# Performance work log

Measured on AMD Instinct MI355X. Metric: run time of the kernel, lower is better.

Reference implementation:

```python
import jax, jax.numpy as jnp
import numpy as np

B, N, C, H, W = 32, 8, 256, 4, 4


def setup_inputs() -> dict:
    key = jax.random.key(0)
    k1, k2 = jax.random.split(key)
    pred = jax.random.normal(k1, (B, N, C, H, W), dtype=jnp.float32)
    gt = jax.random.normal(k2, (B, N, C, H, W), dtype=jnp.float32)
    return {"pred": pred, "gt": gt}


def reference(pred, gt):
    b, n, c, h, w = pred.shape
    M = b * n * h * w
    # (B,N,C,H,W) -> (B,N,H,W,C) -> (M, C)
    p = jnp.transpose(pred, (0, 1, 3, 4, 2)).reshape(M, c)
    # (B,N,C,H,W) -> (C,B,N,H,W) -> (C, M)
    g = jnp.transpose(gt, (2, 0, 1, 3, 4)).reshape(c, M)
    lossmat = p @ g  # (M, M) similarity matrix
    # CrossEntropy with target = arange(M): -mean(log_softmax diag)
    logp = jax.nn.log_softmax(lossmat, axis=1)
    loss = -jnp.mean(jnp.diagonal(logp))
    # accuracy (no grad in original)
    top1 = jnp.argmax(lossmat, axis=1)
    acc = jnp.mean((top1 == jnp.arange(M)).astype(jnp.float32)) * 100.0
    return (loss, acc)
```

## Files before the change

### kernel.cpp

```cpp
#include <hip/hip_runtime.h>
#include <cstdint>

typedef __bf16 bf16x8 __attribute__((ext_vector_type(8)));
typedef float floatx4 __attribute__((ext_vector_type(4)));


#define OFF_X     (0u)
#define OFF_Y     (2u*1024*1024)
#define OFF_PMAX  (4u*1024*1024)
#define OFF_PSUM  (5u*1024*1024)
#define OFF_DIAG  (6u*1024*1024)
#define OFF_LPART (OFF_DIAG + 16384u)
#define OFF_CPART (OFF_LPART + 256u)
#define OFF_CNT   (OFF_CPART + 256u)

#define AS1C(p) ((const __attribute__((address_space(1))) void*)(const void*)(p))
#define AS3(p)  ((__attribute__((address_space(3))) void*)(void*)(p))

__global__ __launch_bounds__(256) void transpose_stage(
    const float* __restrict__ pred, const float* __restrict__ gt,
    unsigned short* __restrict__ Xs, unsigned short* __restrict__ Ys,
    int* __restrict__ cnt) {
  int blk = blockIdx.x;
  const int t = threadIdx.x;
  if (blk == 0 && t < 33) cnt[t] = 0;
  const float* src;
  unsigned short* dst;
  int slab;
  if (blk < 256) { src = pred; dst = Xs; slab = blk; }
  else           { src = gt;   dst = Ys; slab = blk - 256; }
  const float* sb = src + slab * 4096;
  const int rb = slab >> 3, rowhi = slab & 7;
  #pragma unroll
  for (int half = 0; half < 2; ++half) {
    int c_ = half * 256 + t;
    int rowlo = c_ & 15;
    int quad  = (c_ >> 4) & 3;
    int kk    = (c_ >> 6) & 1;
    int s     = c_ >> 7;
    int k0 = s * 64 + kk * 32 + quad * 8;
    unsigned int packed[4];
    #pragma unroll
    for (int jj = 0; jj < 4; ++jj) {
      unsigned int lohi[2];
      #pragma unroll
      for (int e = 0; e < 2; ++e) {
        float f = sb[(k0 + jj * 2 + e) * 16 + rowlo];
        unsigned int u = __float_as_uint(f);
        lohi[e] = (u + 0x7FFFu + ((u >> 16) & 1u)) >> 16;
      }
      packed[jj] = lohi[0] | (lohi[1] << 16);
    }
    unsigned short* o = dst + rb * 32768 +
        (unsigned)(s * 1024 + kk * 512 + rowhi * 64 + quad * 16 + rowlo) * 8;
    uint4 v; v.x = packed[0]; v.y = packed[1]; v.z = packed[2]; v.w = packed[3];
    *reinterpret_cast<uint4*>(o) = v;
  }
}

__global__ __launch_bounds__(512) void gemm_softmax_partial(
    const unsigned short* __restrict__ Xs, const unsigned short* __restrict__ Ys,
    float* __restrict__ pmax, float* __restrict__ psum, float* __restrict__ diag) {
  __shared__ __align__(16) unsigned short As[2][16384];
  __shared__ __align__(16) unsigned short Bs[2][16384];
  const int t = threadIdx.x;
  const int wave = t >> 6, lane = t & 63;
  const int rg = wave >> 2, cg = wave & 3;
  const int h = blockIdx.x;
  const int xcd = h & 7, slot = h >> 3;
  const int bR = ((xcd >> 1) << 2) | (slot & 3);
  const int bC = ((xcd & 1) << 3) | (slot >> 2);
  const unsigned short* Ag = Xs + bR * 65536;
  const unsigned short* Bg = Ys + bC * 65536;

  floatx4 acc[8][4];
  const floatx4 zero = {0.f, 0.f, 0.f, 0.f};
  #pragma unroll
  for (int i = 0; i < 8; ++i)
    #pragma unroll
    for (int j = 0; j < 4; ++j) acc[i][j] = zero;

#define STAGE(BUF, S) do {                                                   \
    _Pragma("unroll") for (int it = 0; it < 4; ++it) {                       \
      int chunk = it * 512 + t;                                 \
      int half = chunk >> 10, w_ = chunk & 1023;                             \
      __builtin_amdgcn_global_load_lds(                                      \
          AS1C(Ag + half * 32768 + (S) * 8192 + w_ * 8),                     \
          AS3(&As[BUF][(unsigned)chunk * 8]), 16, 0, 0);                     \
      __builtin_amdgcn_global_load_lds(                                      \
          AS1C(Bg + half * 32768 + (S) * 8192 + w_ * 8),                     \
          AS3(&Bs[BUF][(unsigned)chunk * 8]), 16, 0, 0);                     \
    }                                                                        \
  } while (0)

#define COMPUTE(BUF) do {                                                    \
    _Pragma("unroll") for (int kk = 0; kk < 2; ++kk) {                       \
      bf16x8 b[4];                                                           \
      _Pragma("unroll") for (int fc = 0; fc < 4; ++fc) {                     \
        int gc = cg * 4 + fc;                                                \
        b[fc] = *reinterpret_cast<const bf16x8*>(                            \
            &Bs[BUF][(unsigned)((gc >> 3) * 8192 + kk * 4096 +               \
                                (gc & 7) * 512 + lane * 8)]);                \
      }                                                                      \
      _Pragma("unroll") for (int fr = 0; fr < 8; ++fr) {                     \
        bf16x8 a = *reinterpret_cast<const bf16x8*>(                         \
            &As[BUF][(unsigned)(rg * 8192 + kk * 4096 + fr * 512 +           \
                                lane * 8)]);                                 \
        _Pragma("unroll") for (int fc = 0; fc < 4; ++fc)                     \
          acc[fr][fc] = __builtin_amdgcn_mfma_f32_16x16x32_bf16(             \
              a, b[fc], acc[fr][fc], 0, 0, 0);                               \
      }                                                                      \
    }                                                                        \
  } while (0)

#define BAR_ACQ(N) do {                                                      \
    asm volatile("s_waitcnt vmcnt(" #N ")" ::: "memory");                    \
    __builtin_amdgcn_s_barrier();                                            \
    asm volatile("" ::: "memory");                                           \
  } while (0)
#define BAR_REL() do {                                                       \
    asm volatile("" ::: "memory");                                           \
    __builtin_amdgcn_s_barrier();                                            \
  } while (0)

  STAGE(0, 0);
  STAGE(1, 1);
  BAR_ACQ(8);
  COMPUTE(0);
  BAR_REL();
  STAGE(0, 2);
  BAR_ACQ(8);
  COMPUTE(1);
  BAR_REL();
  STAGE(1, 3);
  BAR_ACQ(8);
  COMPUTE(0);
  BAR_ACQ(0);
  COMPUTE(1);

#undef STAGE
#undef COMPUTE
#undef BAR_ACQ
#undef BAR_REL

  const int quad = lane >> 4, lc = lane & 15;

  if (bR == bC) {
    #pragma unroll
    for (int fr = 0; fr < 8; ++fr) {
      if (cg == 2 * rg + (fr >> 2)) {
        #pragma unroll
        for (int r = 0; r < 4; ++r)
          if (lc == quad * 4 + r)
            diag[bR * 256 + rg * 128 + fr * 16 + lc] = acc[fr][fr & 3][r];
      }
    }
  }

  #pragma unroll
  for (int fr = 0; fr < 8; ++fr) {
    #pragma unroll
    for (int r = 0; r < 4; ++r) {
      float v0 = acc[fr][0][r], v1 = acc[fr][1][r];
      float v2 = acc[fr][2][r], v3 = acc[fr][3][r];
      float m = fmaxf(fmaxf(v0, v1), fmaxf(v2, v3));
      #pragma unroll
      for (int sh = 1; sh < 16; sh <<= 1) m = fmaxf(m, __shfl_xor(m, sh, 64));
      float ss = __expf(v0 - m) + __expf(v1 - m) +
                 __expf(v2 - m) + __expf(v3 - m);
      #pragma unroll
      for (int sh = 1; sh < 16; sh <<= 1) ss += __shfl_xor(ss, sh, 64);
      if (lc == 0) {
        int grow = bR * 256 + rg * 128 + fr * 16 + quad * 4 + r;
        int p = grow * 64 + bC * 4 + cg;
        pmax[p] = m; psum[p] = ss;
      }
    }
  }
}

__global__ __launch_bounds__(256) void combine_rows(
    const float* __restrict__ pmax, const float* __restrict__ psum,
    const float* __restrict__ diag,
    float* __restrict__ lpart, float* __restrict__ cpart,
    int* __restrict__ cnt, float* __restrict__ out) {
  int row = blockIdx.x * 256 + threadIdx.x;
  const float* pm = pmax + row * 64;
  const float* ps = psum + row * 64;
  float M = -3.4e38f;
  #pragma unroll 8
  for (int b = 0; b < 64; ++b) M = fmaxf(M, pm[b]);
  float S = 0.f;
  #pragma unroll 8
  for (int b = 0; b < 64; ++b) S += ps[b] * __expf(pm[b] - M);
  float d = diag[row];
  float lossr = logf(S) + M - d;
  float corr = (d == M) ? 1.f : 0.f;
  #pragma unroll
  for (int sh = 1; sh < 64; sh <<= 1) {
    lossr += __shfl_xor(lossr, sh, 64);
    corr  += __shfl_xor(corr,  sh, 64);
  }
  __shared__ float ls[4], cs[4];
  int wave = threadIdx.x >> 6, lane = threadIdx.x & 63;
  if (lane == 0) { ls[wave] = lossr; cs[wave] = corr; }
  __syncthreads();
  if (threadIdx.x == 0) {
    lpart[blockIdx.x] = ls[0] + ls[1] + ls[2] + ls[3];
    cpart[blockIdx.x] = cs[0] + cs[1] + cs[2] + cs[3];
    __threadfence();
    if (atomicAdd(cnt, 1) == 15) {
      __threadfence();
      float L = 0.f, C = 0.f;
      for (int i = 0; i < 16; ++i) { L += lpart[i]; C += cpart[i]; }
      out[0] = L * (1.f / 4096.f);
      out[1] = C * (100.f / 4096.f);
    }
  }
}

extern "C" void kernel_launch(void* const* d_in, const int* in_sizes, int n_in,
                              void* d_out, int out_size, void* d_ws, size_t ws_size,
                              hipStream_t stream) {
  const float* pred = (const float*)d_in[0];
  const float* gt   = (const float*)d_in[1];
  char* w = (char*)d_ws;
  unsigned short* Xbf = (unsigned short*)(w + OFF_X);
  unsigned short* Ybf = (unsigned short*)(w + OFF_Y);
  float* pmax  = (float*)(w + OFF_PMAX);
  float* psum  = (float*)(w + OFF_PSUM);
  float* diag  = (float*)(w + OFF_DIAG);
  float* lpart = (float*)(w + OFF_LPART);
  float* cpart = (float*)(w + OFF_CPART);
  int*   cnt   = (int*)(w + OFF_CNT);
  float* out   = (float*)d_out;

  transpose_stage<<<512, 256, 0, stream>>>(pred, gt, Xbf, Ybf, cnt);
  gemm_softmax_partial<<<256, 512, 0, stream>>>(Xbf, Ybf, pmax, psum, diag);
  combine_rows<<<16, 256, 0, stream>>>(pmax, psum, diag, lpart, cpart, cnt, out);
}
```

Baseline: 94.20 us.

## Materialize full similarity matrix and compute softmax in separate combine kernel

The GEMM kernel no longer fuses the per-tile row max/sum-exp reduction. It writes the full 4096x4096 fp32 logits matrix to workspace. A new combine kernel streams each row to compute the max, log-sum-exp, diagonal and argmax match, and a tiny finalize kernel replaces the atomic-counter last-block reduction. This removes shuffle-heavy epilogue work from the GEMM but adds a 64 MB global write and read plus an extra launch.

```diff
diff --git a/kernel.cpp b/kernel.cpp
--- a/kernel.cpp
+++ b/kernel.cpp
@@ -7,23 +7,18 @@
 
 #define OFF_X     (0u)
 #define OFF_Y     (2u*1024*1024)
-#define OFF_PMAX  (4u*1024*1024)
-#define OFF_PSUM  (5u*1024*1024)
-#define OFF_DIAG  (6u*1024*1024)
-#define OFF_LPART (OFF_DIAG + 16384u)
-#define OFF_CPART (OFF_LPART + 256u)
-#define OFF_CNT   (OFF_CPART + 256u)
+#define OFF_LPART (4u*1024*1024)
+#define OFF_CPART (4u*1024*1024 + 4096u)
+#define OFF_LM    (16u*1024*1024)
 
 #define AS1C(p) ((const __attribute__((address_space(1))) void*)(const void*)(p))
 #define AS3(p)  ((__attribute__((address_space(3))) void*)(void*)(p))
 
 __global__ __launch_bounds__(256) void transpose_stage(
     const float* __restrict__ pred, const float* __restrict__ gt,
-    unsigned short* __restrict__ Xs, unsigned short* __restrict__ Ys,
-    int* __restrict__ cnt) {
+    unsigned short* __restrict__ Xs, unsigned short* __restrict__ Ys) {
   int blk = blockIdx.x;
   const int t = threadIdx.x;
-  if (blk == 0 && t < 33) cnt[t] = 0;
   const float* src;
   unsigned short* dst;
   int slab;
@@ -58,9 +53,9 @@
   }
 }
 
-__global__ __launch_bounds__(512) void gemm_softmax_partial(
+__global__ __launch_bounds__(512) void gemm_c(
     const unsigned short* __restrict__ Xs, const unsigned short* __restrict__ Ys,
-    float* __restrict__ pmax, float* __restrict__ psum, float* __restrict__ diag) {
+    float* __restrict__ LM) {
   __shared__ __align__(16) unsigned short As[2][16384];
   __shared__ __align__(16) unsigned short Bs[2][16384];
   const int t = threadIdx.x;
@@ -144,78 +139,71 @@
 #undef BAR_REL
 
   const int quad = lane >> 4, lc = lane & 15;
-
-  if (bR == bC) {
-    #pragma unroll
-    for (int fr = 0; fr < 8; ++fr) {
-      if (cg == 2 * rg + (fr >> 2)) {
-        #pragma unroll
-        for (int r = 0; r < 4; ++r)
-          if (lc == quad * 4 + r)
-            diag[bR * 256 + rg * 128 + fr * 16 + lc] = acc[fr][fr & 3][r];
-      }
-    }
-  }
-
-  #pragma unroll
-  for (int fr = 0; fr < 8; ++fr) {
-    #pragma unroll
-    for (int r = 0; r < 4; ++r) {
-      float v0 = acc[fr][0][r], v1 = acc[fr][1][r];
-      float v2 = acc[fr][2][r], v3 = acc[fr][3][r];
-      float m = fmaxf(fmaxf(v0, v1), fmaxf(v2, v3));
+  float* Cb = LM + (size_t)(bR * 256 + rg * 128 + quad * 4) * 4096 +
+              bC * 256 + cg * 64 + lc;
+  #pragma unroll
+  for (int fr = 0; fr < 8; ++fr)
+    #pragma unroll
+    for (int r = 0; r < 4; ++r)
       #pragma unroll
-      for (int sh = 1; sh < 16; sh <<= 1) m = fmaxf(m, __shfl_xor(m, sh, 64));
-      float ss = __expf(v0 - m) + __expf(v1 - m) +
-                 __expf(v2 - m) + __expf(v3 - m);
-      #pragma unroll
-      for (int sh = 1; sh < 16; sh <<= 1) ss += __shfl_xor(ss, sh, 64);
-      if (lc == 0) {
-        int grow = bR * 256 + rg * 128 + fr * 16 + quad * 4 + r;
-        int p = grow * 64 + bC * 4 + cg;
-        pmax[p] = m; psum[p] = ss;
-      }
-    }
-  }
-}
-
-__global__ __launch_bounds__(256) void combine_rows(
-    const float* __restrict__ pmax, const float* __restrict__ psum,
-    const float* __restrict__ diag,
-    float* __restrict__ lpart, float* __restrict__ cpart,
-    int* __restrict__ cnt, float* __restrict__ out) {
-  int row = blockIdx.x * 256 + threadIdx.x;
-  const float* pm = pmax + row * 64;
-  const float* ps = psum + row * 64;
-  float M = -3.4e38f;
-  #pragma unroll 8
-  for (int b = 0; b < 64; ++b) M = fmaxf(M, pm[b]);
-  float S = 0.f;
-  #pragma unroll 8
-  for (int b = 0; b < 64; ++b) S += ps[b] * __expf(pm[b] - M);
-  float d = diag[row];
-  float lossr = logf(S) + M - d;
-  float corr = (d == M) ? 1.f : 0.f;
-  #pragma unroll
-  for (int sh = 1; sh < 64; sh <<= 1) {
-    lossr += __shfl_xor(lossr, sh, 64);
-    corr  += __shfl_xor(corr,  sh, 64);
+      for (int fc = 0; fc < 4; ++fc)
+        Cb[(size_t)(fr * 16 + r) * 4096 + fc * 16] = acc[fr][fc][r];
+}
+
+__global__ __launch_bounds__(256) void combine_full(
+    const float* __restrict__ LM,
+    float* __restrict__ lpart, float* __restrict__ cpart) {
+  const int t = threadIdx.x;
+  const int wave = t >> 6, lane = t & 63;
+  const int w_global = blockIdx.x * 4 + wave;
+  float lossacc = 0.f, corracc = 0.f;
+  #pragma unroll 1
+  for (int rr = 0; rr < 8; ++rr) {
+    int row = w_global * 8 + rr;
+    const float4* rp = reinterpret_cast<const float4*>(LM + (size_t)row * 4096);
+    float4 f[16];
+    #pragma unroll
+    for (int it = 0; it < 16; ++it) f[it] = rp[it * 64 + lane];
+    float m = -3.4e38f;
+    #pragma unroll
+    for (int it = 0; it < 16; ++it)
+      m = fmaxf(m, fmaxf(fmaxf(f[it].x, f[it].y), fmaxf(f[it].z, f[it].w)));
+    #pragma unroll
+    for (int sh = 1; sh < 64; sh <<= 1) m = fmaxf(m, __shfl_xor(m, sh, 64));
+    float ss = 0.f;
+    #pragma unroll
+    for (int it = 0; it < 16; ++it)
+      ss += __expf(f[it].x - m) + __expf(f[it].y - m) +
+            __expf(f[it].z - m) + __expf(f[it].w - m);
+    #pragma unroll
+    for (int sh = 1; sh < 64; sh <<= 1) ss += __shfl_xor(ss, sh, 64);
+    float d = LM[(size_t)row * 4096 + row];
+    lossacc += logf(ss) + m - d;
+    corracc += (d == m) ? 1.f : 0.f;
   }
   __shared__ float ls[4], cs[4];
-  int wave = threadIdx.x >> 6, lane = threadIdx.x & 63;
-  if (lane == 0) { ls[wave] = lossr; cs[wave] = corr; }
+  if (lane == 0) { ls[wave] = lossacc; cs[wave] = corracc; }
   __syncthreads();
-  if (threadIdx.x == 0) {
+  if (t == 0) {
     lpart[blockIdx.x] = ls[0] + ls[1] + ls[2] + ls[3];
     cpart[blockIdx.x] = cs[0] + cs[1] + cs[2] + cs[3];
-    __threadfence();
-    if (atomicAdd(cnt, 1) == 15) {
-      __threadfence();
-      float L = 0.f, C = 0.f;
-      for (int i = 0; i < 16; ++i) { L += lpart[i]; C += cpart[i]; }
-      out[0] = L * (1.f / 4096.f);
-      out[1] = C * (100.f / 4096.f);
-    }
+  }
+}
+
+__global__ void finalize(const float* __restrict__ lpart,
+                         const float* __restrict__ cpart,
+                         float* __restrict__ out) {
+  int t = threadIdx.x;
+  float l = lpart[t] + lpart[t + 64];
+  float c = cpart[t] + cpart[t + 64];
+  #pragma unroll
+  for (int sh = 1; sh < 64; sh <<= 1) {
+    l += __shfl_xor(l, sh, 64);
+    c += __shfl_xor(c, sh, 64);
+  }
+  if (t == 0) {
+    out[0] = l * (1.f / 4096.f);
+    out[1] = c * (100.f / 4096.f);
   }
 }
 
@@ -227,15 +215,13 @@
   char* w = (char*)d_ws;
   unsigned short* Xbf = (unsigned short*)(w + OFF_X);
   unsigned short* Ybf = (unsigned short*)(w + OFF_Y);
-  float* pmax  = (float*)(w + OFF_PMAX);
-  float* psum  = (float*)(w + OFF_PSUM);
-  float* diag  = (float*)(w + OFF_DIAG);
   float* lpart = (float*)(w + OFF_LPART);
   float* cpart = (float*)(w + OFF_CPART);
-  int*   cnt   = (int*)(w + OFF_CNT);
+  float* LM    = (float*)(w + OFF_LM);
   float* out   = (float*)d_out;
 
-  transpose_stage<<<512, 256, 0, stream>>>(pred, gt, Xbf, Ybf, cnt);
-  gemm_softmax_partial<<<256, 512, 0, stream>>>(Xbf, Ybf, pmax, psum, diag);
-  combine_rows<<<16, 256, 0, stream>>>(pmax, psum, diag, lpart, cpart, cnt, out);
-}
+  transpose_stage<<<512, 256, 0, stream>>>(pred, gt, Xbf, Ybf);
+  gemm_c<<<256, 512, 0, stream>>>(Xbf, Ybf, LM);
+  combine_full<<<128, 256, 0, stream>>>(LM, lpart, cpart);
+  finalize<<<1, 64, 0, stream>>>(lpart, cpart, out);
+}
```

New measurement: 95.81 us. About the same (+1.7%).
